# Kernel tuning notes

Measured on AMD Instinct MI355X. Metric: run time of the kernel, lower is better.

The kernel has to match this reference:

```python
import jax, jax.numpy as jnp
import numpy as np

B, A, Bdim, C = 8, 256, 256, 64  # batch, height a, width b, channels
F = Bdim // 2 + 1                 # rfft width


def setup_inputs() -> dict:
    key = jax.random.key(0)
    k1, k2, k3 = jax.random.split(key, 3)
    x = jax.random.normal(k1, (B, A, Bdim, C), dtype=jnp.float32)
    # complex spectral weight stored as two float planes, shape [a, f, C]
    scale = 1.0 / (A * Bdim)
    w_real = jax.random.normal(k2, (A, F, C), dtype=jnp.float32) * scale
    w_imag = jax.random.normal(k3, (A, F, C), dtype=jnp.float32) * scale
    return {"x": x, "w_real": w_real, "w_imag": w_imag}


def reference(x, w_real, w_imag):
    # Depthwise FNO-style spectral conv:
    #   y[b,:,:,c] = irfft2( rfft2(x[b,:,:,c]) * W[:,:,c] )
    # The CUDA version packs BHWC -> planar [B*C,a,b], runs cuFFT R2C,
    # multiplies by W [a,f,C] elementwise in the spectrum, C2R, and scales
    # by 1/(a*b) (cuFFT is unnormalized). jnp.fft.irfft2 already applies
    # the 1/(a*b) normalization, so layouts/scale fold away here.
    a, b = x.shape[1], x.shape[2]
    W = jax.lax.complex(w_real, w_imag)          # [a, f, C] complex64
    Xf = jnp.fft.rfft2(x, axes=(1, 2))           # [B, a, f, C]
    y = jnp.fft.irfft2(Xf * W[None], s=(a, b), axes=(1, 2))
    return y.astype(x.dtype)
```

## Files before the change

### kernel.cpp

```cpp
#include <hip/hip_runtime.h>
#include <math.h>

#define NB 8
#define NA 256
#define NBD 256
#define NC 64
#define NF 129

struct alignas(8) cpx { float re, im; };

union H2U { uint u; _Float16 h[2]; };
__device__ __forceinline__ uint pkc(float re, float im){
  H2U x; x.h[0] = (_Float16)re; x.h[1] = (_Float16)im; return x.u;
}
__device__ __forceinline__ cpx unpkc(uint u){
  H2U x; x.u = u; cpx c; c.re = (float)x.h[0]; c.im = (float)x.h[1]; return c;
}

__device__ __forceinline__ cpx cmul(cpx a, cpx b){
  cpx r;
  r.re = fmaf(a.re, b.re, -(a.im * b.im));
  r.im = fmaf(a.re, b.im,  a.im * b.re);
  return r;
}

__device__ __forceinline__ int PHY(int n, int g){
  return (n << 5) | ((g + n + (n >> 4)) & 31);
}

__device__ __forceinline__ int PHYS(int r, int c){
  int p = ((r & 1) ^ ((r >> 4) & 1)) << 4;
  int s = (((r >> 1) + (r >> 5)) & 3) << 2;
  return ((r >> 1) << 5) | p | ((c & 12) ^ s) | (c & 3);
}

__global__ __launch_bounds__(256) void k0w_pack(const float* __restrict__ wre,
                                                const float* __restrict__ wim,
                                                uint* __restrict__ wp,
                                                float2* __restrict__ tw){
  const int blk = blockIdx.x;
  const int f = blk >> 2, h = blk & 3;
  const int tid = threadIdx.x;
  if (blk == 0){
    double ang = 6.283185307179586476925286766559 * (double)tid / 256.0;
    tw[tid] = make_float2((float)cos(ang), (float)sin(ang));
  }
  const int c = tid & 15, kb = tid >> 4;
  uint* dst = wp + (size_t)blk * 4096;
  #pragma unroll
  for (int it = 0; it < 16; ++it){
    int ka = kb + 16*it;
    size_t src = ((size_t)ka*NF + f)*64 + h*16 + c;
    dst[ka*16 + c] = pkc(wre[src] * 256.0f, wim[src] * 256.0f);
  }
}

template<int SIGN>
__device__ __forceinline__ void fft16(cpx a[16]){
  cpx tmp;
  #define SW(i,j) tmp = a[i]; a[i] = a[j]; a[j] = tmp;
  SW(1,8) SW(2,4) SW(3,12) SW(5,10) SW(7,14) SW(11,13)
  #undef SW
  const float CT[8] = {1.f, 0.92387953251128674f, 0.70710678118654752f, 0.38268343236508977f,
                       0.f, -0.38268343236508977f, -0.70710678118654752f, -0.92387953251128674f};
  const float ST[8] = {0.f, 0.38268343236508977f, 0.70710678118654752f, 0.92387953251128674f,
                       1.f, 0.92387953251128674f, 0.70710678118654752f, 0.38268343236508977f};
  #pragma unroll
  for (int s = 1; s <= 4; ++s){
    const int m = 1 << s, half = m >> 1, str = 16 >> s;
    #pragma unroll
    for (int k = 0; k < 16; k += m){
      #pragma unroll
      for (int j = 0; j < half; ++j){
        cpx w; w.re = CT[j*str]; w.im = (float)SIGN * ST[j*str];
        cpx t = cmul(a[k+j+half], w);
        cpx u = a[k+j];
        a[k+j].re      = u.re + t.re; a[k+j].im      = u.im + t.im;
        a[k+j+half].re = u.re - t.re; a[k+j+half].im = u.im - t.im;
      }
    }
  }
}

template<int SIGN>
__device__ __forceinline__ void fft256_col(cpx* __restrict__ tile, int g, int t,
                                           const float2* __restrict__ tw){
  cpx a[16];
  #pragma unroll
  for (int n1 = 0; n1 < 16; ++n1) a[n1] = tile[PHY(16*n1 + t, g)];
  fft16<SIGN>(a);
  #pragma unroll
  for (int k1 = 1; k1 < 16; ++k1){
    float2 tv = tw[(t * k1) & 255];
    cpx w; w.re = tv.x; w.im = (SIGN < 0) ? -tv.y : tv.y;
    a[k1] = cmul(a[k1], w);
  }
  #pragma unroll
  for (int k1 = 0; k1 < 16; ++k1) tile[PHY(16*k1 + t, g)] = a[k1];
  __builtin_amdgcn_wave_barrier();

  cpx b[16];
  #pragma unroll
  for (int n2 = 0; n2 < 16; ++n2) b[n2] = tile[PHY(16*t + n2, g)];
  fft16<SIGN>(b);
  __builtin_amdgcn_wave_barrier();
  #pragma unroll
  for (int k2 = 0; k2 < 16; ++k2) tile[PHY(t + 16*k2, g)] = b[k2];
  __syncthreads();
}


__global__ __launch_bounds__(512) void k1_rfft_b(const float* __restrict__ x,
                                                 uint2* __restrict__ mid_p2,
                                                 const float2* __restrict__ tw){
  __shared__ cpx tile[256*32];
  const int tid = threadIdx.x;
  const int blk = blockIdx.x;
  const int bb = blk >> 8, a = blk & 255;
  const int g = tid >> 4, t = tid & 15;

  const float4* src = (const float4*)(x + (size_t)blk * (NBD * NC));
  #pragma unroll
  for (int it = 0; it < 8; ++it){
    int idx = it*512 + tid;
    int j = idx >> 4, q = idx & 15;
    float4 v = src[idx];
    cpx p0; p0.re = v.x; p0.im = v.y;
    cpx p1; p1.re = v.z; p1.im = v.w;
    tile[PHY(j, 2*q)]   = p0;
    tile[PHY(j, 2*q+1)] = p1;
  }
  __syncthreads();

  fft256_col<-1>(tile, g, t, tw);

  for (int it = 0; it < 9; ++it){
    int idx = it*512 + tid;
    if (idx < NF*32){
      int k = idx >> 5, gg = idx & 31;
      cpx zk = tile[PHY(k, gg)];
      cpx zm = tile[PHY((256 - k) & 255, gg)];
      float Ar = 0.5f*(zk.re + zm.re);
      float Ai = 0.5f*(zk.im - zm.im);
      float Br = 0.5f*(zk.im + zm.im);
      float Bi = 0.5f*(zm.re - zk.re);
      size_t o = ((((size_t)bb*NF + k)*4 + (gg >> 3))*256 + a)*8 + (gg & 7);
      uint2 pv; pv.x = pkc(Ar, Ai); pv.y = pkc(Br, Bi);
      mid_p2[o] = pv;
    }
  }
}

__global__ __launch_bounds__(256)
void k2_fft_a_mul(uint* __restrict__ mid_u,
                  const uint* __restrict__ wp,
                  const float2* __restrict__ tw){
  __shared__ uint tile_u[256*16];
  __shared__ uint wtile[256*16];
  const int tid = threadIdx.x;
  const int blk = blockIdx.x;
  const int f = blk >> 5;
  const int bb = (blk >> 2) & 7, h = blk & 3;
  const int g = tid >> 4, t = tid & 15;

  uint* base_u = mid_u + ((((size_t)bb*NF + f)*4 + h) << 12);
  const uint* wslab = wp + ((size_t)(f*4 + h) << 12);

  const uint4* base4 = (const uint4*)base_u;
  const uint4* w4    = (const uint4*)wslab;
  #pragma unroll
  for (int it = 0; it < 4; ++it){
    int idx = it*256 + tid;
    int r = idx >> 2, q = idx & 3;
    uint4 v  = base4[idx];
    uint4 wv = w4[idx];
    *(uint4*)&tile_u[PHYS(r, 4*q)] = v;
    *(uint4*)&wtile[PHYS(r, 4*q)]  = wv;
  }
  __syncthreads();

  cpx b[16];
  #pragma unroll
  for (int n1 = 0; n1 < 16; ++n1) b[n1] = unpkc(tile_u[PHYS(16*n1 + t, g)]);
  fft16<-1>(b);
  #pragma unroll
  for (int k1 = 1; k1 < 16; ++k1){
    float2 tv = tw[(t * k1) & 255];
    cpx w; w.re = tv.x; w.im = -tv.y;
    b[k1] = cmul(b[k1], w);
  }

  #pragma unroll
  for (int k1 = 0; k1 < 16; ++k1) tile_u[PHYS(16*k1 + t, g)] = pkc(b[k1].re, b[k1].im);
  __builtin_amdgcn_wave_barrier();
  #pragma unroll
  for (int n2 = 0; n2 < 16; ++n2) b[n2] = unpkc(tile_u[PHYS(16*t + n2, g)]);

  fft16<-1>(b);

  #pragma unroll
  for (int k2 = 0; k2 < 16; ++k2){
    cpx w = unpkc(wtile[PHYS(t + 16*k2, g)]);
    b[k2] = cmul(b[k2], w);
  }

  fft16<1>(b);
  #pragma unroll
  for (int k1 = 1; k1 < 16; ++k1){
    float2 tv = tw[(t * k1) & 255];
    cpx w; w.re = tv.x; w.im = tv.y;
    b[k1] = cmul(b[k1], w);
  }

  __builtin_amdgcn_wave_barrier();
  #pragma unroll
  for (int k1 = 0; k1 < 16; ++k1) tile_u[PHYS(16*k1 + t, g)] = pkc(b[k1].re, b[k1].im);
  __builtin_amdgcn_wave_barrier();
  #pragma unroll
  for (int n2 = 0; n2 < 16; ++n2) b[n2] = unpkc(tile_u[PHYS(16*t + n2, g)]);

  fft16<1>(b);
  #pragma unroll
  for (int k2 = 0; k2 < 16; ++k2) tile_u[PHYS(t + 16*k2, g)] = pkc(b[k2].re, b[k2].im);
  __syncthreads();

  uint4* ob = (uint4*)base_u;
  #pragma unroll
  for (int it = 0; it < 4; ++it){
    int idx = it*256 + tid;
    int r = idx >> 2, q = idx & 3;
    ob[idx] = *(const uint4*)&tile_u[PHYS(r, 4*q)];
  }
}

__global__ __launch_bounds__(512) void k3_irfft_b(const uint2* __restrict__ mid_p2,
                                                  float2* __restrict__ y2,
                                                  const float2* __restrict__ tw){
  __shared__ cpx tile[256*32];
  const int tid = threadIdx.x;
  const int blk = blockIdx.x;
  const int bb = blk >> 8, a = blk & 255;
  const int g = tid >> 4, t = tid & 15;

  for (int it = 0; it < 9; ++it){
    int idx = it*512 + tid;
    if (idx < NF*32){
      int f = idx >> 5, gg = idx & 31;
      size_t o = ((((size_t)bb*NF + f)*4 + (gg >> 3))*256 + a)*8 + (gg & 7);
      uint2 pv = mid_p2[o];
      cpx A = unpkc(pv.x), B = unpkc(pv.y);
      cpx sd;
      if (f == 0 || f == 128){
        sd.re = A.re;
        sd.im = B.re;
      } else {
        sd.re = A.re - B.im; sd.im = A.im + B.re;
      }
      tile[PHY(f, gg)] = sd;
      if (f >= 1 && f <= 127){
        cpx se; se.re = A.re + B.im; se.im = B.re - A.im;
        tile[PHY(256 - f, gg)] = se;
      }
    }
  }
  __syncthreads();

  fft256_col<+1>(tile, g, t, tw);

  const float SC = 5.9604644775390625e-08f;
  float2* dst = y2 + (size_t)blk * (256*32);
  #pragma unroll
  for (int it = 0; it < 16; ++it){
    int idx = it*512 + tid;
    int n = idx >> 5, gg = idx & 31;
    cpx v = tile[PHY(n, gg)];
    float2 o; o.x = v.re * SC; o.y = v.im * SC;
    dst[(size_t)n*32 + gg] = o;
  }
}

extern "C" void kernel_launch(void* const* d_in, const int* in_sizes, int n_in,
                              void* d_out, int out_size, void* d_ws, size_t ws_size,
                              hipStream_t stream){
  const float* x   = (const float*)d_in[0];
  const float* wre = (const float*)d_in[1];
  const float* wim = (const float*)d_in[2];

  float2* tw   = (float2*)d_ws;
  uint*   wpck = (uint*)d_ws + 512;
  uint*   midu = wpck + (size_t)NF*4*4096;

  k0w_pack    <<<NF*4,   256, 0, stream>>>(wre, wim, wpck, tw);
  k1_rfft_b   <<<NB*NA,  512, 0, stream>>>(x, (uint2*)midu, tw);
  k2_fft_a_mul<<<NF*32,  256, 0, stream>>>(midu, wpck, tw);
  k3_irfft_b  <<<NB*NA,  512, 0, stream>>>((const uint2*)midu, (float2*)d_out, tw);
}
```

Before: 164.7 us.

## Make rfft-b kernel persistent with register prefetch of next row

The first FFT kernel now launches 512 blocks, and each block loops over four rows instead of handling one row per block. While the current row's FFT runs out of shared memory, the next row's input is prefetched into registers, so global load latency overlaps with compute. The cost is higher register pressure from holding eight float4 values, and fewer blocks to hide latency on a GPU with many CUs.

```diff
diff --git a/kernel.cpp b/kernel.cpp
--- a/kernel.cpp
+++ b/kernel.cpp
@@ -115,39 +115,55 @@
                                                  const float2* __restrict__ tw){
   __shared__ cpx tile[256*32];
   const int tid = threadIdx.x;
-  const int blk = blockIdx.x;
-  const int bb = blk >> 8, a = blk & 255;
   const int g = tid >> 4, t = tid & 15;
 
-  const float4* src = (const float4*)(x + (size_t)blk * (NBD * NC));
-  #pragma unroll
-  for (int it = 0; it < 8; ++it){
-    int idx = it*512 + tid;
-    int j = idx >> 4, q = idx & 15;
-    float4 v = src[idx];
-    cpx p0; p0.re = v.x; p0.im = v.y;
-    cpx p1; p1.re = v.z; p1.im = v.w;
-    tile[PHY(j, 2*q)]   = p0;
-    tile[PHY(j, 2*q+1)] = p1;
-  }
-  __syncthreads();
-
-  fft256_col<-1>(tile, g, t, tw);
-
-  for (int it = 0; it < 9; ++it){
-    int idx = it*512 + tid;
-    if (idx < NF*32){
-      int k = idx >> 5, gg = idx & 31;
-      cpx zk = tile[PHY(k, gg)];
-      cpx zm = tile[PHY((256 - k) & 255, gg)];
-      float Ar = 0.5f*(zk.re + zm.re);
-      float Ai = 0.5f*(zk.im - zm.im);
-      float Br = 0.5f*(zk.im + zm.im);
-      float Bi = 0.5f*(zm.re - zk.re);
-      size_t o = ((((size_t)bb*NF + k)*4 + (gg >> 3))*256 + a)*8 + (gg & 7);
-      uint2 pv; pv.x = pkc(Ar, Ai); pv.y = pkc(Br, Bi);
-      mid_p2[o] = pv;
-    }
+  int row = blockIdx.x;
+  float4 v[8];
+  {
+    const float4* src = (const float4*)(x + (size_t)row * (NBD * NC));
+    #pragma unroll
+    for (int it = 0; it < 8; ++it) v[it] = src[it*512 + tid];
+  }
+
+  for (int r = 0; r < 4; ++r){
+    #pragma unroll
+    for (int it = 0; it < 8; ++it){
+      int idx = it*512 + tid;
+      int j = idx >> 4, q = idx & 15;
+      cpx p0; p0.re = v[it].x; p0.im = v[it].y;
+      cpx p1; p1.re = v[it].z; p1.im = v[it].w;
+      tile[PHY(j, 2*q)]   = p0;
+      tile[PHY(j, 2*q+1)] = p1;
+    }
+    __syncthreads();
+
+    if (r < 3){
+      const float4* nsrc = (const float4*)(x + (size_t)(row + 512) * (NBD * NC));
+      #pragma unroll
+      for (int it = 0; it < 8; ++it) v[it] = nsrc[it*512 + tid];
+    }
+
+    fft256_col<-1>(tile, g, t, tw);
+
+    const int bb = row >> 8, a = row & 255;
+    for (int it9 = 0; it9 < 9; ++it9){
+      int idx = it9*512 + tid;
+      if (idx < NF*32){
+        int k = idx >> 5, gg = idx & 31;
+        cpx zk = tile[PHY(k, gg)];
+        cpx zm = tile[PHY((256 - k) & 255, gg)];
+        float Ar = 0.5f*(zk.re + zm.re);
+        float Ai = 0.5f*(zk.im - zm.im);
+        float Br = 0.5f*(zk.im + zm.im);
+        float Bi = 0.5f*(zm.re - zk.re);
+        size_t o = ((((size_t)bb*NF + k)*4 + (gg >> 3))*256 + a)*8 + (gg & 7);
+        uint2 pv; pv.x = pkc(Ar, Ai); pv.y = pkc(Br, Bi);
+        mid_p2[o] = pv;
+      }
+    }
+    __syncthreads();
+
+    row += 512;
   }
 }
 
@@ -291,7 +307,7 @@
   uint*   midu = wpck + (size_t)NF*4*4096;
 
   k0w_pack    <<<NF*4,   256, 0, stream>>>(wre, wim, wpck, tw);
-  k1_rfft_b   <<<NB*NA,  512, 0, stream>>>(x, (uint2*)midu, tw);
+  k1_rfft_b   <<<512,    512, 0, stream>>>(x, (uint2*)midu, tw);
   k2_fft_a_mul<<<NF*32,  256, 0, stream>>>(midu, wpck, tw);
   k3_irfft_b  <<<NB*NA,  512, 0, stream>>>((const uint2*)midu, (float2*)d_out, tw);
 }
```

Measured after the change: 167.3 us. About the same (+1.6%).
